# Kernel tuning notes

Measured on AMD Instinct MI355X. Metric: run time of the kernel, lower is better.

The kernel has to match this reference:

```python
import jax, jax.numpy as jnp
from jax import lax
import numpy as np

# dims
B, T, W, D = 8, 24, 48, 512
H = 8            # n_head
E = D // H       # head dim = 64
DI = 2 * D       # mamba d_inner (expand=2) = 1024
S = 64           # d_state
R = 32           # dt_rank = ceil(512/16)
KC = 4           # mamba depthwise conv kernel
DFF = 2048       # ffn hidden
L = T * W


def setup_inputs() -> dict:
    key = jax.random.key(0)
    ks = jax.random.split(key, 32)
    def g(i, shape, s=0.02):
        return jax.random.normal(ks[i], shape, dtype=jnp.float32) * s
    inp = {
        "x": jax.random.normal(ks[0], (B, T, W, D), dtype=jnp.float32),
        "slf_attn_mask": jnp.zeros((B, L), dtype=bool),
        # attention projections (torch Linear convention: y = x @ W.T + b)
        "Wq": g(1, (D, D)), "bq": jnp.zeros((D,), jnp.float32),
        "Wk": g(2, (D, D)), "bk": jnp.zeros((D,), jnp.float32),
        "Wv": g(3, (D, D)), "bv": jnp.zeros((D,), jnp.float32),
        "Wo": g(4, (D, D)), "bo": jnp.zeros((D,), jnp.float32),
        # mamba params
        "in_proj_w": g(5, (2 * DI, D)),
        "conv_w": g(6, (DI, KC), 0.1),
        "conv_b": jnp.zeros((DI,), jnp.float32),
        "x_proj_w": g(7, (R + 2 * S, DI)),
        "dt_proj_w": g(8, (DI, R), 0.1),
        "dt_proj_b": jnp.full((DI,), -3.0, jnp.float32),  # softplus -> small dt
        "A_log": jnp.broadcast_to(jnp.log(jnp.arange(1, S + 1, dtype=jnp.float32)), (DI, S)).copy(),
        "D_ssm": jnp.ones((DI,), jnp.float32),
        "out_proj_w": g(9, (D, DI)),
        # hybrid LayerNorm
        "ln1_g": jnp.ones((D,), jnp.float32), "ln1_b": jnp.zeros((D,), jnp.float32),
        # FFN (pre-norm)
        "ffn_w1": g(10, (DFF, D)), "ffn_b1": jnp.zeros((DFF,), jnp.float32),
        "ffn_w2": g(11, (D, DFF)), "ffn_b2": jnp.zeros((D,), jnp.float32),
        "ln2_g": jnp.ones((D,), jnp.float32), "ln2_b": jnp.zeros((D,), jnp.float32),
    }
    return inp


def _layernorm(x, g, b, eps):
    m = jnp.mean(x, -1, keepdims=True)
    v = jnp.mean(jnp.square(x - m), -1, keepdims=True)
    return (x - m) * lax.rsqrt(v + eps) * g + b


def _attention(xf, mask, Wq, bq, Wk, bk, Wv, bv, Wo, bo):
    # xf: [B, L, D]; mask: [B, L] bool (True = masked)
    b, l, _ = xf.shape
    q = (xf @ Wq.T + bq).reshape(b, l, H, E)
    k = (xf @ Wk.T + bk).reshape(b, l, H, E)
    v = (xf @ Wv.T + bv).reshape(b, l, H, E)
    scale = 1.0 / jnp.sqrt(jnp.float32(E))
    scores = jnp.einsum('blhe,bshe->bhls', q, k)                 # [B,H,L,L]
    scores = jnp.where(mask[:, None, None, :], -jnp.inf, scores)
    probs = jax.nn.softmax(scale * scores, axis=-1)
    out = jnp.einsum('bhls,bshe->blhe', probs, v).reshape(b, l, D)
    return out @ Wo.T + bo


def _mamba(xf, in_proj_w, conv_w, conv_b, x_proj_w, dt_proj_w, dt_proj_b, A_log, D_ssm, out_proj_w):
    # xf: [B, L, D]
    b, l, _ = xf.shape
    xz = xf @ in_proj_w.T                  # [B,L,2*DI]
    u, z = jnp.split(xz, 2, axis=-1)
    # causal depthwise conv1d, kernel KC
    up = jnp.pad(u, ((0, 0), (KC - 1, 0), (0, 0)))
    uc = conv_b + sum(up[:, k:k + l, :] * conv_w[:, k] for k in range(KC))
    u = jax.nn.silu(uc)                    # [B,L,DI]
    xdbc = u @ x_proj_w.T                  # [B,L,R+2S]
    dt_r, Bm, Cm = jnp.split(xdbc, [R, R + S], axis=-1)
    delta = jax.nn.softplus(dt_r @ dt_proj_w.T + dt_proj_b)   # [B,L,DI]
    A = -jnp.exp(A_log)                    # [DI,S]

    def step(h, xs):
        dt_t, u_t, B_t, C_t = xs           # [B,DI],[B,DI],[B,S],[B,S]
        dA = jnp.exp(dt_t[:, :, None] * A)                       # [B,DI,S]
        h = h * dA + (dt_t * u_t)[:, :, None] * B_t[:, None, :]
        y = jnp.einsum('bds,bs->bd', h, C_t)
        return h, y

    xs = (delta.transpose(1, 0, 2), u.transpose(1, 0, 2),
          Bm.transpose(1, 0, 2), Cm.transpose(1, 0, 2))
    h0 = jnp.zeros((b, DI, S), dtype=xf.dtype)
    _, ys = lax.scan(step, h0, xs)
    y = ys.transpose(1, 0, 2) + u * D_ssm  # [B,L,DI]
    y = y * jax.nn.silu(z)
    return y @ out_proj_w.T


def _forward(x, slf_attn_mask, Wq, bq, Wk, bk, Wv, bv, Wo, bo,
             in_proj_w, conv_w, conv_b, x_proj_w, dt_proj_w, dt_proj_b,
             A_log, D_ssm, out_proj_w, ln1_g, ln1_b,
             ffn_w1, ffn_b1, ffn_w2, ffn_b2, ln2_g, ln2_b):
    b, t, w, d = x.shape
    xf = x.reshape(b, t * w, d)
    x_attn = _attention(xf, slf_attn_mask, Wq, bq, Wk, bk, Wv, bv, Wo, bo)
    x_mamba = _mamba(xf, in_proj_w, conv_w, conv_b, x_proj_w, dt_proj_w,
                     dt_proj_b, A_log, D_ssm, out_proj_w)
    h = xf + x_attn + x_mamba
    h = _layernorm(h, ln1_g, ln1_b, 1e-5)
    # pre-norm FFN with residual
    hn = _layernorm(h, ln2_g, ln2_b, 1e-6)
    ff = jax.nn.gelu(hn @ ffn_w1.T + ffn_b1, approximate=False) @ ffn_w2.T + ffn_b2
    out = h + ff
    return out.reshape(b, t, w, d)


def reference(x, slf_attn_mask, Wq, bq, Wk, bk, Wv, bv, Wo, bo,
              in_proj_w, conv_w, conv_b, x_proj_w, dt_proj_w, dt_proj_b,
              A_log, D_ssm, out_proj_w, ln1_g, ln1_b,
              ffn_w1, ffn_b1, ffn_w2, ffn_b2, ln2_g, ln2_b):
    return _forward(x, slf_attn_mask, Wq, bq, Wk, bk, Wv, bv, Wo, bo,
                    in_proj_w, conv_w, conv_b, x_proj_w, dt_proj_w, dt_proj_b,
                    A_log, D_ssm, out_proj_w, ln1_g, ln1_b,
                    ffn_w1, ffn_b1, ffn_w2, ffn_b2, ln2_g, ln2_b)
```

## Files before the change

kernel.cpp:

```cpp
#include <hip/hip_runtime.h>
#include <hip/hip_bf16.h>
#include <math.h>

#define BB 8
#define DD 512
#define HH 8
#define EE 64
#define DI 1024
#define SS 64
#define RR 32
#define KCONV 4
#define DFF 2048
#define LL 1152
#define ML (BB*LL)
#define XS (RR + 2*SS)
#define ZSTR 2048

typedef short bf16x8 __attribute__((ext_vector_type(8)));
typedef float f32x4 __attribute__((ext_vector_type(4)));
typedef unsigned short u16x4 __attribute__((ext_vector_type(4)));

#define GLD_LDS(g, l) \
  __builtin_amdgcn_global_load_lds((const __attribute__((address_space(1))) void*)(g), \
                                   (__attribute__((address_space(3))) void*)(l), 16, 0, 0)

__device__ __forceinline__ float bf2f(unsigned short u) {
  return __uint_as_float(((unsigned)u) << 16);
}

template<int IMM>
__device__ __forceinline__ float swz(float x) {
  return __uint_as_float((unsigned)__builtin_amdgcn_ds_swizzle((int)__float_as_uint(x), IMM));
}

__global__ __launch_bounds__(256) void cvt_bf16(
    const float* __restrict__ s, __hip_bfloat16* __restrict__ d, int n)
{
  const int i = (blockIdx.x * 256 + threadIdx.x) * 4;
  if (i + 3 < n) {
    const float4 v = *(const float4*)(s + i);
    __hip_bfloat16 t[4] = {__float2bfloat16(v.x), __float2bfloat16(v.y),
                           __float2bfloat16(v.z), __float2bfloat16(v.w)};
    *(ushort4*)(d + i) = *(const ushort4*)t;
  } else {
    for (int k = i; k < n; ++k) d[k] = __float2bfloat16(s[k]);
  }
}

__global__ __launch_bounds__(256) void gemm_mfma(
    const __hip_bfloat16* __restrict__ A, int lda,
    const __hip_bfloat16* __restrict__ W,
    const float* __restrict__ bias,
    const float* __restrict__ res,
    void* __restrict__ Cv, void* __restrict__ Cv2,
    int M, int N, int K, int act, int mode)
{
  __shared__ __align__(16) __hip_bfloat16 As[128 * 32];
  __shared__ __align__(16) __hip_bfloat16 Ws[128 * 32];
  const int tid = threadIdx.x;
  const int wid = tid >> 6, lane = tid & 63;
  const int wr = wid >> 1, wc = wid & 1;
  const int m0 = blockIdx.y << 7, n0 = blockIdx.x << 7;
  const int r1 = tid >> 2;
  const int c1 = (tid & 3) << 3;

  const __hip_bfloat16* ga0 = A + (size_t)(m0 + r1) * lda + c1;
  const __hip_bfloat16* ga1 = A + (size_t)(m0 + 64 + r1) * lda + c1;
  const __hip_bfloat16* gw0 = W + (size_t)(n0 + r1) * K + c1;
  const __hip_bfloat16* gw1 = W + (size_t)(n0 + 64 + r1) * K + c1;
  char* lA0 = (char*)As + wid * 1024;
  char* lA1 = lA0 + 4096;
  char* lW0 = (char*)Ws + wid * 1024;
  char* lW1 = lW0 + 4096;

  f32x4 acc[4][4];
#pragma unroll
  for (int i = 0; i < 4; ++i)
#pragma unroll
    for (int j = 0; j < 4; ++j) acc[i][j] = (f32x4){0.f, 0.f, 0.f, 0.f};

  const int fm = lane & 15;
  const int q8 = (lane >> 4) << 3;

  for (int kt = 0; kt < K; kt += 32) {
    __syncthreads();
    GLD_LDS(ga0, lA0); GLD_LDS(ga1, lA1);
    GLD_LDS(gw0, lW0); GLD_LDS(gw1, lW1);
    ga0 += 32; ga1 += 32; gw0 += 32; gw1 += 32;
    __syncthreads();

    bf16x8 af[4], wf[4];
#pragma unroll
    for (int i = 0; i < 4; ++i)
      af[i] = *(const bf16x8*)((const short*)As + (wr * 64 + i * 16 + fm) * 32 + q8);
#pragma unroll
    for (int j = 0; j < 4; ++j)
      wf[j] = *(const bf16x8*)((const short*)Ws + (wc * 64 + j * 16 + fm) * 32 + q8);
#pragma unroll
    for (int i = 0; i < 4; ++i)
#pragma unroll
      for (int j = 0; j < 4; ++j)
        acc[i][j] = __builtin_amdgcn_mfma_f32_16x16x32_bf16(af[i], wf[j], acc[i][j], 0, 0, 0);
  }

  const int rquad = (lane >> 4) << 2;
#pragma unroll
  for (int j = 0; j < 4; ++j) {
    const int n = n0 + wc * 64 + j * 16 + fm;
    if (n < N) {
      const float bv = bias ? bias[n] : 0.f;
#pragma unroll
      for (int i = 0; i < 4; ++i) {
        const int mb = m0 + wr * 64 + i * 16 + rquad;
#pragma unroll
        for (int r = 0; r < 4; ++r) {
          const int m = mb + r;
          float v = acc[i][j][r] + bv;
          if (act == 1) v = 0.5f * v * (1.f + erff(v * 0.70710678118654752f));
          else if (act == 2) v = fmaxf(v, 0.f) + log1pf(expf(-fabsf(v)));
          if (mode == 3) {
            if (n < 1024) {
              ((__hip_bfloat16*)Cv)[(size_t)m * 1024 + n] = __float2bfloat16(v);
            } else {
              const int e = n - 1024;
              const int bb2 = m / LL;
              const int key = m - bb2 * LL;
              ((__hip_bfloat16*)Cv2)[((size_t)(bb2 * HH + (e >> 6)) * EE + (e & 63)) * LL + key] =
                  __float2bfloat16(v);
            }
          } else {
            const size_t off = (size_t)m * N + n;
            if (res) v += res[off];
            if (mode == 1) ((__hip_bfloat16*)Cv)[off] = __float2bfloat16(v);
            else ((float*)Cv)[off] = v;
          }
        }
      }
    }
  }
}

__global__ __launch_bounds__(256) void conv_silu(
    const __hip_bfloat16* __restrict__ xz, const float* __restrict__ cw,
    const float* __restrict__ cb, __hip_bfloat16* __restrict__ uout)
{
  const size_t idx = (size_t)blockIdx.x * 256 + threadIdx.x;
  if (idx >= (size_t)ML * DI) return;
  const int di = (int)(idx & (DI - 1));
  const int row = (int)(idx >> 10);
  const int t = row % LL;
  float acc = cb[di];
#pragma unroll
  for (int k = 0; k < KCONV; ++k) {
    if (t - (KCONV - 1) + k >= 0)
      acc = fmaf((float)xz[(size_t)(row - (KCONV - 1 - k)) * ZSTR + di],
                 cw[di * KCONV + k], acc);
  }
  uout[idx] = __float2bfloat16(acc / (1.f + __expf(-acc)));
}

#define SLOAD(P_, t0_) { _Pragma("unroll") for (int j = 0; j < 4; ++j) { \
    P_##_dt[j] = dp[(size_t)((t0_)+j)*DI]; \
    P_##_u[j]  = bf2f(ubp[(size_t)((t0_)+j)*DI]); \
    P_##_B[j]  = *(const u16x4*)(Bp + (size_t)((t0_)+j)*XS); \
    P_##_C[j]  = *(const u16x4*)(Cp + (size_t)((t0_)+j)*XS); } }

#define SSTEP(P_, j, idx) { \
    const float dtu = P_##_dt[j] * P_##_u[j]; \
    h0 = fmaf(h0, __expf(P_##_dt[j] * Av[0]), dtu * bf2f(P_##_B[j][0])); \
    h1 = fmaf(h1, __expf(P_##_dt[j] * Av[1]), dtu * bf2f(P_##_B[j][1])); \
    h2 = fmaf(h2, __expf(P_##_dt[j] * Av[2]), dtu * bf2f(P_##_B[j][2])); \
    h3 = fmaf(h3, __expf(P_##_dt[j] * Av[3]), dtu * bf2f(P_##_B[j][3])); \
    float part = h0 * bf2f(P_##_C[j][0]); \
    part = fmaf(h1, bf2f(P_##_C[j][1]), part); \
    part = fmaf(h2, bf2f(P_##_C[j][2]), part); \
    part = fmaf(h3, bf2f(P_##_C[j][3]), part); \
    Pp[(idx)] = part; }

#define SCOMP(P_, base_) { \
    SSTEP(P_, 0, (base_)+0) SSTEP(P_, 1, (base_)+1) \
    SSTEP(P_, 2, (base_)+2) SSTEP(P_, 3, (base_)+3) }

__global__ __launch_bounds__(256) void scan_kernel(
    const float* __restrict__ delta, const __hip_bfloat16* __restrict__ ubf,
    const __hip_bfloat16* __restrict__ xz, const __hip_bfloat16* __restrict__ xdbc,
    const float* __restrict__ A_log, const float* __restrict__ D_ssm,
    __hip_bfloat16* __restrict__ y)
{
  const int wv = (int)((blockIdx.x * 256 + threadIdx.x) >> 6);
  const int lane = threadIdx.x & 63;
  const int c = lane >> 4;
  const int s4 = lane & 15;
  const int g = (wv << 2) + c;
  const int b = g >> 10;
  const int di = g & (DI - 1);
  float Av[4];
#pragma unroll
  for (int kk = 0; kk < 4; ++kk)
    Av[kk] = -__expf(A_log[di * SS + (s4 << 2) + kk]);
  const float Dd = D_ssm[di];
  const size_t rb = (size_t)b * LL;
  const float* __restrict__ dp = delta + rb * DI + di;
  const unsigned short* __restrict__ ubp = (const unsigned short*)ubf + rb * DI + di;
  const unsigned short* __restrict__ zbp = (const unsigned short*)xz + rb * ZSTR + DI + di;
  const unsigned short* __restrict__ Bp = (const unsigned short*)xdbc + rb * XS + RR + (s4 << 2);
  const unsigned short* __restrict__ Cp = Bp + SS;
  __hip_bfloat16* __restrict__ yp = y + rb * DI + di;

  float h0 = 0.f, h1 = 0.f, h2 = 0.f, h3 = 0.f;
  float Pp[16];
  float a_dt[4], a_u[4]; u16x4 a_B[4], a_C[4];
  float b_dt[4], b_u[4]; u16x4 b_B[4], b_C[4];
  float c_dt[4], c_u[4]; u16x4 c_B[4], c_C[4];
  float d_dt[4], d_u[4]; u16x4 d_B[4], d_C[4];

  float u_e = bf2f(ubp[(size_t)s4 * DI]);
  float z_e = bf2f(zbp[(size_t)s4 * ZSTR]);

  SLOAD(a, 0) SLOAD(b, 4) SLOAD(c, 8)
  for (int t0 = 0; t0 < LL; t0 += 16) {
    SLOAD(d, t0 + 12)
    SCOMP(a, 0)
    if (t0 + 16 < LL) SLOAD(a, t0 + 16)
    SCOMP(b, 4)
    float u_n = 0.f, z_n = 0.f;
    if (t0 + 16 < LL) {
      u_n = bf2f(ubp[(size_t)(t0 + 16 + s4) * DI]);
      z_n = bf2f(zbp[(size_t)(t0 + 16 + s4) * ZSTR]);
    }
    if (t0 + 20 < LL) SLOAD(b, t0 + 20)
    SCOMP(c, 8)
    if (t0 + 24 < LL) SLOAD(c, t0 + 24)
    SCOMP(d, 12)

#pragma unroll
    for (int k2 = 0; k2 < 8; ++k2) {
      const float mn = (s4 & 1) ? Pp[2*k2+1] : Pp[2*k2];
      const float ot = (s4 & 1) ? Pp[2*k2]   : Pp[2*k2+1];
      Pp[k2] = mn + swz<0x041F>(ot);
    }
#pragma unroll
    for (int k2 = 0; k2 < 4; ++k2) {
      const float mn = (s4 & 2) ? Pp[2*k2+1] : Pp[2*k2];
      const float ot = (s4 & 2) ? Pp[2*k2]   : Pp[2*k2+1];
      Pp[k2] = mn + swz<0x081F>(ot);
    }
#pragma unroll
    for (int k2 = 0; k2 < 2; ++k2) {
      const float mn = (s4 & 4) ? Pp[2*k2+1] : Pp[2*k2];
      const float ot = (s4 & 4) ? Pp[2*k2]   : Pp[2*k2+1];
      Pp[k2] = mn + swz<0x101F>(ot);
    }
    {
      const float mn = (s4 & 8) ? Pp[1] : Pp[0];
      const float ot = (s4 & 8) ? Pp[0] : Pp[1];
      Pp[0] = mn + swz<0x201F>(ot);
    }

    const float yv = (Pp[0] + u_e * Dd) * (z_e / (1.f + __expf(-z_e)));
    yp[(size_t)(t0 + s4) * DI] = __float2bfloat16(yv);
    u_e = u_n; z_e = z_n;
  }
}

__global__ __launch_bounds__(256) void attn_mfma(
    const __hip_bfloat16* __restrict__ qk,
    const __hip_bfloat16* __restrict__ vtg, __hip_bfloat16* __restrict__ og)
{
  __shared__ __align__(16) __hip_bfloat16 Qs[64][72];
  __shared__ __align__(16) __hip_bfloat16 Ks[64][72];
  __shared__ __align__(16) __hip_bfloat16 Vts[64][72];
  __shared__ __align__(16) __hip_bfloat16 Ps[4][16][72];
  const int tid = threadIdx.x;
  const int w = tid >> 6, lane = tid & 63;
  const int bh = blockIdx.y;
  const int b = bh >> 3, hh = bh & 7;
  const int q0 = blockIdx.x << 6;
  const size_t qbase = (size_t)b * LL * 1024 + (size_t)hh * EE;
  const size_t vtbase = (size_t)bh * EE * LL;
  const size_t obase = (size_t)b * LL * DD + (size_t)hh * EE;

  const int srow = tid >> 2, sch = (tid & 3) << 4;
  {
    const __hip_bfloat16* src = qk + qbase + (size_t)(q0 + srow) * 1024 + sch;
    *(uint4*)&Qs[srow][sch]     = *(const uint4*)src;
    *(uint4*)&Qs[srow][sch + 8] = *(const uint4*)(src + 8);
  }
  __syncthreads();

  const int fm = lane & 15;
  const int q8 = (lane >> 4) << 3;
  bf16x8 af0 = *(const bf16x8*)&Qs[w * 16 + fm][q8];
  bf16x8 af1 = *(const bf16x8*)&Qs[w * 16 + fm][32 + q8];

  f32x4 oacc[4];
  float m_i[4], l_i[4];
#pragma unroll
  for (int r = 0; r < 4; ++r) { m_i[r] = -INFINITY; l_i[r] = 0.f; }
#pragma unroll
  for (int j = 0; j < 4; ++j) oacc[j] = (f32x4){0.f, 0.f, 0.f, 0.f};

  for (int kt = 0; kt < LL / 64; ++kt) {
    const int k0 = kt << 6;
    __syncthreads();
    {
      const __hip_bfloat16* ksrc = qk + qbase + 512 + (size_t)(k0 + srow) * 1024 + sch;
      const __hip_bfloat16* vsrc = vtg + vtbase + (size_t)srow * LL + k0 + sch;
      *(uint4*)&Ks[srow][sch]      = *(const uint4*)ksrc;
      *(uint4*)&Ks[srow][sch + 8]  = *(const uint4*)(ksrc + 8);
      *(uint4*)&Vts[srow][sch]     = *(const uint4*)vsrc;
      *(uint4*)&Vts[srow][sch + 8] = *(const uint4*)(vsrc + 8);
    }
    __syncthreads();

    f32x4 sacc[4];
#pragma unroll
    for (int j = 0; j < 4; ++j) sacc[j] = (f32x4){0.f, 0.f, 0.f, 0.f};
#pragma unroll
    for (int j = 0; j < 4; ++j) {
      bf16x8 kf0 = *(const bf16x8*)&Ks[j * 16 + fm][q8];
      bf16x8 kf1 = *(const bf16x8*)&Ks[j * 16 + fm][32 + q8];
      sacc[j] = __builtin_amdgcn_mfma_f32_16x16x32_bf16(af0, kf0, sacc[j], 0, 0, 0);
      sacc[j] = __builtin_amdgcn_mfma_f32_16x16x32_bf16(af1, kf1, sacc[j], 0, 0, 0);
    }

    float alpha[4];
#pragma unroll
    for (int r = 0; r < 4; ++r) {
#pragma unroll
      for (int j = 0; j < 4; ++j) sacc[j][r] *= 0.125f;
      float mt = fmaxf(fmaxf(sacc[0][r], sacc[1][r]), fmaxf(sacc[2][r], sacc[3][r]));
      mt = fmaxf(mt, swz<0x041F>(mt)); mt = fmaxf(mt, swz<0x081F>(mt));
      mt = fmaxf(mt, swz<0x101F>(mt)); mt = fmaxf(mt, swz<0x201F>(mt));
      const float mn = fmaxf(m_i[r], mt);
      alpha[r] = __expf(m_i[r] - mn);
      m_i[r] = mn;
      float p[4], rs = 0.f;
#pragma unroll
      for (int j = 0; j < 4; ++j) { p[j] = __expf(sacc[j][r] - mn); rs += p[j]; }
      rs += swz<0x041F>(rs); rs += swz<0x081F>(rs);
      rs += swz<0x101F>(rs); rs += swz<0x201F>(rs);
      l_i[r] = l_i[r] * alpha[r] + rs;
      const int qrow = ((lane >> 4) << 2) + r;
#pragma unroll
      for (int j = 0; j < 4; ++j)
        Ps[w][qrow][j * 16 + fm] = __float2bfloat16(p[j]);
    }
#pragma unroll
    for (int j = 0; j < 4; ++j)
#pragma unroll
      for (int r = 0; r < 4; ++r) oacc[j][r] *= alpha[r];

    bf16x8 pf0 = *(const bf16x8*)&Ps[w][fm][q8];
    bf16x8 pf1 = *(const bf16x8*)&Ps[w][fm][32 + q8];
#pragma unroll
    for (int j = 0; j < 4; ++j) {
      bf16x8 v0 = *(const bf16x8*)&Vts[j * 16 + fm][q8];
      bf16x8 v1 = *(const bf16x8*)&Vts[j * 16 + fm][32 + q8];
      oacc[j] = __builtin_amdgcn_mfma_f32_16x16x32_bf16(pf0, v0, oacc[j], 0, 0, 0);
      oacc[j] = __builtin_amdgcn_mfma_f32_16x16x32_bf16(pf1, v1, oacc[j], 0, 0, 0);
    }
  }

#pragma unroll
  for (int r = 0; r < 4; ++r) {
    const float inv = 1.f / l_i[r];
    const int qq = q0 + w * 16 + ((lane >> 4) << 2) + r;
#pragma unroll
    for (int j = 0; j < 4; ++j)
      og[obase + (size_t)qq * DD + j * 16 + fm] = __float2bfloat16(oacc[j][r] * inv);
  }
}

__device__ __forceinline__ float block_sum512(float val, float* sm)
{
#pragma unroll
  for (int off = 32; off; off >>= 1) val += __shfl_xor(val, off, 64);
  const int wid = threadIdx.x >> 6;
  __syncthreads();
  if ((threadIdx.x & 63) == 0) sm[wid] = val;
  __syncthreads();
  return sm[0] + sm[1] + sm[2] + sm[3];
}

__global__ __launch_bounds__(256) void ln_fused(
    const float* __restrict__ xf, const float* __restrict__ ao,
    const float* __restrict__ mo,
    const float* __restrict__ g1, const float* __restrict__ b1,
    const float* __restrict__ g2, const float* __restrict__ b2,
    float* __restrict__ hout, __hip_bfloat16* __restrict__ hnout)
{
  __shared__ float sm[4];
  const size_t base = (size_t)blockIdx.x * DD;
  const int t = threadIdx.x;
  const float v0 = xf[base + t] + ao[base + t] + mo[base + t];
  const float v1 = xf[base + 256 + t] + ao[base + 256 + t] + mo[base + 256 + t];
  const float mean = block_sum512(v0 + v1, sm) * (1.f / DD);
  const float d0 = v0 - mean, d1 = v1 - mean;
  const float var = block_sum512(d0 * d0 + d1 * d1, sm) * (1.f / DD);
  const float rstd = rsqrtf(var + 1e-5f);
  const float h0 = d0 * rstd * g1[t] + b1[t];
  const float h1 = d1 * rstd * g1[t + 256] + b1[t + 256];
  hout[base + t] = h0;
  hout[base + 256 + t] = h1;
  const float mean2 = block_sum512(h0 + h1, sm) * (1.f / DD);
  const float e0 = h0 - mean2, e1 = h1 - mean2;
  const float var2 = block_sum512(e0 * e0 + e1 * e1, sm) * (1.f / DD);
  const float rstd2 = rsqrtf(var2 + 1e-6f);
  hnout[base + t] = __float2bfloat16(e0 * rstd2 * g2[t] + b2[t]);
  hnout[base + 256 + t] = __float2bfloat16(e1 * rstd2 * g2[t + 256] + b2[t + 256]);
}

extern "C" void kernel_launch(void* const* d_in, const int* in_sizes, int n_in,
                              void* d_out, int out_size, void* d_ws, size_t ws_size,
                              hipStream_t stream)
{
  const float* x         = (const float*)d_in[0];
  const float* Wq        = (const float*)d_in[2];
  const float* bq        = (const float*)d_in[3];
  const float* Wk        = (const float*)d_in[4];
  const float* bk        = (const float*)d_in[5];
  const float* Wv        = (const float*)d_in[6];
  const float* bv        = (const float*)d_in[7];
  const float* Wo        = (const float*)d_in[8];
  const float* bo        = (const float*)d_in[9];
  const float* in_proj_w = (const float*)d_in[10];
  const float* conv_w    = (const float*)d_in[11];
  const float* conv_b    = (const float*)d_in[12];
  const float* x_proj_w  = (const float*)d_in[13];
  const float* dt_proj_w = (const float*)d_in[14];
  const float* dt_proj_b = (const float*)d_in[15];
  const float* A_log     = (const float*)d_in[16];
  const float* D_ssm     = (const float*)d_in[17];
  const float* out_proj_w= (const float*)d_in[18];
  const float* ln1_g     = (const float*)d_in[19];
  const float* ln1_b     = (const float*)d_in[20];
  const float* ffn_w1    = (const float*)d_in[21];
  const float* ffn_b1    = (const float*)d_in[22];
  const float* ffn_w2    = (const float*)d_in[23];
  const float* ffn_b2    = (const float*)d_in[24];
  const float* ln2_g     = (const float*)d_in[25];
  const float* ln2_b     = (const float*)d_in[26];
  float* out = (float*)d_out;

  float* ws = (float*)d_ws;
  const size_t OF_XBF = 2506752;
  const size_t OF_XZ  = OF_XBF + 2359296;
  const size_t OF_UBF = OF_XZ + 9437184;
  const size_t OF_XD  = OF_UBF + 4718592;
  const size_t OF_DF  = OF_XD + 737280;
  const size_t OF_YB  = OF_DF + 9437184;
  const size_t OF_QB  = OF_YB + 4718592;

  __hip_bfloat16* wbf     = (__hip_bfloat16*)ws;
  __hip_bfloat16* xbf     = (__hip_bfloat16*)(ws + OF_XBF);
  __hip_bfloat16* hnbf    = (__hip_bfloat16*)(ws + OF_XBF);
  __hip_bfloat16* xz      = (__hip_bfloat16*)(ws + OF_XZ);
  __hip_bfloat16* qkbuf   = (__hip_bfloat16*)(ws + OF_XZ);
  __hip_bfloat16* vtbf    = (__hip_bfloat16*)(ws + OF_XZ + 4718592);
  __hip_bfloat16* ubf     = (__hip_bfloat16*)(ws + OF_UBF);
  float*          aobuf   = ws + OF_UBF;
  __hip_bfloat16* xdbc_bf = (__hip_bfloat16*)(ws + OF_XD);
  float*          deltab  = ws + OF_DF;
  __hip_bfloat16* attnbf  = (__hip_bfloat16*)(ws + OF_DF);
  float*          mambab  = ws + OF_DF + 2359296;
  __hip_bfloat16* ffbf    = (__hip_bfloat16*)(ws + OF_DF);
  __hip_bfloat16* ybf     = (__hip_bfloat16*)(ws + OF_YB);
  float*          hbuf    = ws + OF_YB;
  float*          qkvbias = ws + OF_QB;

  const size_t w_inproj = 0;
  const size_t w_xproj  = 1048576;
  const size_t w_dt     = 1310720;
  const size_t w_out    = 1343488;
  const size_t w_q      = 1867776;
  const size_t w_o      = 2654208;
  const size_t w_f1     = 2916352;
  const size_t w_f2     = 3964928;

  const dim3 thr(256);
#define CVT(src, dst, n) cvt_bf16<<<dim3(((n)/4 + 255)/256), thr, 0, stream>>>(src, dst, n)
#define GEMM(Abf, lda_, Woff, Bptr, Rptr, Cptr, C2ptr, N_, K_, act_, md_) \
  gemm_mfma<<<dim3((N_ + 127)/128, ML/128), thr, 0, stream>>>( \
      Abf, lda_, wbf + (Woff), Bptr, Rptr, (void*)(Cptr), (void*)(C2ptr), ML, N_, K_, act_, md_)

  hipMemsetAsync((void*)(wbf + w_xproj + (size_t)160 * 1024), 0, (size_t)96 * 1024 * 2, stream);
  CVT(in_proj_w, wbf + w_inproj, 1048576);
  CVT(x_proj_w,  wbf + w_xproj,  163840);
  CVT(dt_proj_w, wbf + w_dt,     32768);
  CVT(out_proj_w,wbf + w_out,    524288);
  CVT(Wq,        wbf + w_q,           262144);
  CVT(Wk,        wbf + w_q + 262144,  262144);
  CVT(Wv,        wbf + w_q + 524288,  262144);
  CVT(Wo,        wbf + w_o,      262144);
  CVT(ffn_w1,    wbf + w_f1,     1048576);
  CVT(ffn_w2,    wbf + w_f2,     1048576);
  CVT(x,         xbf,            ML * DD);
  hipMemcpyAsync(qkvbias,        bq, 512 * sizeof(float), hipMemcpyDeviceToDevice, stream);
  hipMemcpyAsync(qkvbias + 512,  bk, 512 * sizeof(float), hipMemcpyDeviceToDevice, stream);
  hipMemcpyAsync(qkvbias + 1024, bv, 512 * sizeof(float), hipMemcpyDeviceToDevice, stream);

  GEMM(xbf, DD, w_inproj, nullptr, nullptr, xz, nullptr, 2 * DI, DD, 0, 1);
  conv_silu<<<dim3((ML * DI) / 256), thr, 0, stream>>>(xz, conv_w, conv_b, ubf);
  GEMM(ubf, DI, w_xproj, nullptr, nullptr, xdbc_bf, nullptr, XS, DI, 0, 1);
  GEMM(xdbc_bf, XS, w_dt, dt_proj_b, nullptr, deltab, nullptr, DI, RR, 2, 0);
  scan_kernel<<<dim3(512), thr, 0, stream>>>(
      deltab, ubf, xz, xdbc_bf, A_log, D_ssm, ybf);
  GEMM(ybf, DI, w_out, nullptr, nullptr, mambab, nullptr, DD, DI, 0, 0);

  GEMM(xbf, DD, w_q, qkvbias, nullptr, qkbuf, vtbf, 3 * DD, DD, 0, 3);
  attn_mfma<<<dim3(LL / 64, BB * HH), thr, 0, stream>>>(qkbuf, vtbf, attnbf);
  GEMM(attnbf, DD, w_o, bo, nullptr, aobuf, nullptr, DD, DD, 0, 0);

  ln_fused<<<dim3(ML), thr, 0, stream>>>(x, aobuf, mambab, ln1_g, ln1_b,
                                         ln2_g, ln2_b, hbuf, hnbf);

  GEMM(hnbf, DD, w_f1, ffn_b1, nullptr, ffbf, nullptr, DFF, DD, 1, 1);
  GEMM(ffbf, DFF, w_f2, ffn_b2, hbuf, out, nullptr, DD, DFF, 0, 0);
#undef GEMM
#undef CVT
}
```

Baseline: 1.042 ms.

## Co-launch scan and attention in one kernel and fuse out-proj with Wo GEMM

Merges the selective scan and attention kernels into a single launch whose blocks split by index, so the latency-bound scan (512 blocks) overlaps with attention work. Both write into one concatenated bf16 buffer (mamba y in columns 0-1023, attention output in 1024-1535), letting out_proj and Wo run as one K=1536 GEMM with packed weights; this drops one GEMM and one fp32 intermediate from the LayerNorm input. Delta is now stored in bf16, halving its traffic at some precision cost. The merged kernel carries attention's LDS footprint into scan blocks, which may limit occupancy.

Result: no change. 1.036 ms (-0.6%).

```diff
diff --git a/kernel.cpp b/kernel.cpp
--- a/kernel.cpp
+++ b/kernel.cpp
@@ -15,6 +15,7 @@
 #define ML (BB*LL)
 #define XS (RR + 2*SS)
 #define ZSTR 2048
+#define YSTR 1536
 
 typedef short bf16x8 __attribute__((ext_vector_type(8)));
 typedef float f32x4 __attribute__((ext_vector_type(4)));
@@ -45,6 +46,16 @@
   } else {
     for (int k = i; k < n; ++k) d[k] = __float2bfloat16(s[k]);
   }
+}
+
+__global__ __launch_bounds__(256) void cvt_pack(
+    const float* __restrict__ s, __hip_bfloat16* __restrict__ d,
+    int srclen, int dststride, int dstoff, int total)
+{
+  const int i = blockIdx.x * 256 + threadIdx.x;
+  if (i >= total) return;
+  const int r = i / srclen, c = i - r * srclen;
+  d[(size_t)r * dststride + dstoff + c] = __float2bfloat16(s[i]);
 }
 
 __global__ __launch_bounds__(256) void gemm_mfma(
@@ -160,7 +171,7 @@
 }
 
 #define SLOAD(P_, t0_) { _Pragma("unroll") for (int j = 0; j < 4; ++j) { \
-    P_##_dt[j] = dp[(size_t)((t0_)+j)*DI]; \
+    P_##_dt[j] = bf2f(dp[(size_t)((t0_)+j)*DI]); \
     P_##_u[j]  = bf2f(ubp[(size_t)((t0_)+j)*DI]); \
     P_##_B[j]  = *(const u16x4*)(Bp + (size_t)((t0_)+j)*XS); \
     P_##_C[j]  = *(const u16x4*)(Cp + (size_t)((t0_)+j)*XS); } }
@@ -181,104 +192,105 @@
     SSTEP(P_, 0, (base_)+0) SSTEP(P_, 1, (base_)+1) \
     SSTEP(P_, 2, (base_)+2) SSTEP(P_, 3, (base_)+3) }
 
-__global__ __launch_bounds__(256) void scan_kernel(
-    const float* __restrict__ delta, const __hip_bfloat16* __restrict__ ubf,
+__global__ __launch_bounds__(256) void scan_attn(
+    const __hip_bfloat16* __restrict__ delta, const __hip_bfloat16* __restrict__ ubf,
     const __hip_bfloat16* __restrict__ xz, const __hip_bfloat16* __restrict__ xdbc,
     const float* __restrict__ A_log, const float* __restrict__ D_ssm,
-    __hip_bfloat16* __restrict__ y)
-{
-  const int wv = (int)((blockIdx.x * 256 + threadIdx.x) >> 6);
-  const int lane = threadIdx.x & 63;
-  const int c = lane >> 4;
-  const int s4 = lane & 15;
-  const int g = (wv << 2) + c;
-  const int b = g >> 10;
-  const int di = g & (DI - 1);
-  float Av[4];
-#pragma unroll
-  for (int kk = 0; kk < 4; ++kk)
-    Av[kk] = -__expf(A_log[di * SS + (s4 << 2) + kk]);
-  const float Dd = D_ssm[di];
-  const size_t rb = (size_t)b * LL;
-  const float* __restrict__ dp = delta + rb * DI + di;
-  const unsigned short* __restrict__ ubp = (const unsigned short*)ubf + rb * DI + di;
-  const unsigned short* __restrict__ zbp = (const unsigned short*)xz + rb * ZSTR + DI + di;
-  const unsigned short* __restrict__ Bp = (const unsigned short*)xdbc + rb * XS + RR + (s4 << 2);
-  const unsigned short* __restrict__ Cp = Bp + SS;
-  __hip_bfloat16* __restrict__ yp = y + rb * DI + di;
-
-  float h0 = 0.f, h1 = 0.f, h2 = 0.f, h3 = 0.f;
-  float Pp[16];
-  float a_dt[4], a_u[4]; u16x4 a_B[4], a_C[4];
-  float b_dt[4], b_u[4]; u16x4 b_B[4], b_C[4];
-  float c_dt[4], c_u[4]; u16x4 c_B[4], c_C[4];
-  float d_dt[4], d_u[4]; u16x4 d_B[4], d_C[4];
-
-  float u_e = bf2f(ubp[(size_t)s4 * DI]);
-  float z_e = bf2f(zbp[(size_t)s4 * ZSTR]);
-
-  SLOAD(a, 0) SLOAD(b, 4) SLOAD(c, 8)
-  for (int t0 = 0; t0 < LL; t0 += 16) {
-    SLOAD(d, t0 + 12)
-    SCOMP(a, 0)
-    if (t0 + 16 < LL) SLOAD(a, t0 + 16)
-    SCOMP(b, 4)
-    float u_n = 0.f, z_n = 0.f;
-    if (t0 + 16 < LL) {
-      u_n = bf2f(ubp[(size_t)(t0 + 16 + s4) * DI]);
-      z_n = bf2f(zbp[(size_t)(t0 + 16 + s4) * ZSTR]);
-    }
-    if (t0 + 20 < LL) SLOAD(b, t0 + 20)
-    SCOMP(c, 8)
-    if (t0 + 24 < LL) SLOAD(c, t0 + 24)
-    SCOMP(d, 12)
-
-#pragma unroll
-    for (int k2 = 0; k2 < 8; ++k2) {
-      const float mn = (s4 & 1) ? Pp[2*k2+1] : Pp[2*k2];
-      const float ot = (s4 & 1) ? Pp[2*k2]   : Pp[2*k2+1];
-      Pp[k2] = mn + swz<0x041F>(ot);
-    }
-#pragma unroll
-    for (int k2 = 0; k2 < 4; ++k2) {
-      const float mn = (s4 & 2) ? Pp[2*k2+1] : Pp[2*k2];
-      const float ot = (s4 & 2) ? Pp[2*k2]   : Pp[2*k2+1];
-      Pp[k2] = mn + swz<0x081F>(ot);
-    }
-#pragma unroll
-    for (int k2 = 0; k2 < 2; ++k2) {
-      const float mn = (s4 & 4) ? Pp[2*k2+1] : Pp[2*k2];
-      const float ot = (s4 & 4) ? Pp[2*k2]   : Pp[2*k2+1];
-      Pp[k2] = mn + swz<0x101F>(ot);
-    }
-    {
-      const float mn = (s4 & 8) ? Pp[1] : Pp[0];
-      const float ot = (s4 & 8) ? Pp[0] : Pp[1];
-      Pp[0] = mn + swz<0x201F>(ot);
-    }
-
-    const float yv = (Pp[0] + u_e * Dd) * (z_e / (1.f + __expf(-z_e)));
-    yp[(size_t)(t0 + s4) * DI] = __float2bfloat16(yv);
-    u_e = u_n; z_e = z_n;
-  }
-}
-
-__global__ __launch_bounds__(256) void attn_mfma(
-    const __hip_bfloat16* __restrict__ qk,
-    const __hip_bfloat16* __restrict__ vtg, __hip_bfloat16* __restrict__ og)
+    const __hip_bfloat16* __restrict__ qk, const __hip_bfloat16* __restrict__ vtg,
+    __hip_bfloat16* __restrict__ yattn)
 {
   __shared__ __align__(16) __hip_bfloat16 Qs[64][72];
   __shared__ __align__(16) __hip_bfloat16 Ks[64][72];
   __shared__ __align__(16) __hip_bfloat16 Vts[64][72];
   __shared__ __align__(16) __hip_bfloat16 Ps[4][16][72];
   const int tid = threadIdx.x;
+
+  if (blockIdx.x < 512) {
+    const int wv = (int)((blockIdx.x * 256 + tid) >> 6);
+    const int lane = tid & 63;
+    const int c = lane >> 4;
+    const int s4 = lane & 15;
+    const int g = (wv << 2) + c;
+    const int b = g >> 10;
+    const int di = g & (DI - 1);
+    float Av[4];
+#pragma unroll
+    for (int kk = 0; kk < 4; ++kk)
+      Av[kk] = -__expf(A_log[di * SS + (s4 << 2) + kk]);
+    const float Dd = D_ssm[di];
+    const size_t rb = (size_t)b * LL;
+    const unsigned short* __restrict__ dp = (const unsigned short*)delta + rb * DI + di;
+    const unsigned short* __restrict__ ubp = (const unsigned short*)ubf + rb * DI + di;
+    const unsigned short* __restrict__ zbp = (const unsigned short*)xz + rb * ZSTR + DI + di;
+    const unsigned short* __restrict__ Bp = (const unsigned short*)xdbc + rb * XS + RR + (s4 << 2);
+    const unsigned short* __restrict__ Cp = Bp + SS;
+    __hip_bfloat16* __restrict__ yp = yattn + rb * YSTR + di;
+
+    float h0 = 0.f, h1 = 0.f, h2 = 0.f, h3 = 0.f;
+    float Pp[16];
+    float a_dt[4], a_u[4]; u16x4 a_B[4], a_C[4];
+    float b_dt[4], b_u[4]; u16x4 b_B[4], b_C[4];
+    float c_dt[4], c_u[4]; u16x4 c_B[4], c_C[4];
+    float d_dt[4], d_u[4]; u16x4 d_B[4], d_C[4];
+
+    float u_e = bf2f(ubp[(size_t)s4 * DI]);
+    float z_e = bf2f(zbp[(size_t)s4 * ZSTR]);
+
+    SLOAD(a, 0) SLOAD(b, 4) SLOAD(c, 8)
+    for (int t0 = 0; t0 < LL; t0 += 16) {
+      SLOAD(d, t0 + 12)
+      SCOMP(a, 0)
+      if (t0 + 16 < LL) SLOAD(a, t0 + 16)
+      SCOMP(b, 4)
+      float u_n = 0.f, z_n = 0.f;
+      if (t0 + 16 < LL) {
+        u_n = bf2f(ubp[(size_t)(t0 + 16 + s4) * DI]);
+        z_n = bf2f(zbp[(size_t)(t0 + 16 + s4) * ZSTR]);
+      }
+      if (t0 + 20 < LL) SLOAD(b, t0 + 20)
+      SCOMP(c, 8)
+      if (t0 + 24 < LL) SLOAD(c, t0 + 24)
+      SCOMP(d, 12)
+
+#pragma unroll
+      for (int k2 = 0; k2 < 8; ++k2) {
+        const float mn = (s4 & 1) ? Pp[2*k2+1] : Pp[2*k2];
+        const float ot = (s4 & 1) ? Pp[2*k2]   : Pp[2*k2+1];
+        Pp[k2] = mn + swz<0x041F>(ot);
+      }
+#pragma unroll
+      for (int k2 = 0; k2 < 4; ++k2) {
+        const float mn = (s4 & 2) ? Pp[2*k2+1] : Pp[2*k2];
+        const float ot = (s4 & 2) ? Pp[2*k2]   : Pp[2*k2+1];
+        Pp[k2] = mn + swz<0x081F>(ot);
+      }
+#pragma unroll
+      for (int k2 = 0; k2 < 2; ++k2) {
+        const float mn = (s4 & 4) ? Pp[2*k2+1] : Pp[2*k2];
+        const float ot = (s4 & 4) ? Pp[2*k2]   : Pp[2*k2+1];
+        Pp[k2] = mn + swz<0x101F>(ot);
+      }
+      {
+        const float mn = (s4 & 8) ? Pp[1] : Pp[0];
+        const float ot = (s4 & 8) ? Pp[0] : Pp[1];
+        Pp[0] = mn + swz<0x201F>(ot);
+      }
+
+      const float yv = (Pp[0] + u_e * Dd) * (z_e / (1.f + __expf(-z_e)));
+      yp[(size_t)(t0 + s4) * YSTR] = __float2bfloat16(yv);
+      u_e = u_n; z_e = z_n;
+    }
+    return;
+  }
+
+  const int abid = blockIdx.x - 512;
   const int w = tid >> 6, lane = tid & 63;
-  const int bh = blockIdx.y;
+  const int bh = abid / (LL / 64);
+  const int qtile = abid - bh * (LL / 64);
   const int b = bh >> 3, hh = bh & 7;
-  const int q0 = blockIdx.x << 6;
+  const int q0 = qtile << 6;
   const size_t qbase = (size_t)b * LL * 1024 + (size_t)hh * EE;
   const size_t vtbase = (size_t)bh * EE * LL;
-  const size_t obase = (size_t)b * LL * DD + (size_t)hh * EE;
 
   const int srow = tid >> 2, sch = (tid & 3) << 4;
   {
@@ -368,7 +380,8 @@
     const int qq = q0 + w * 16 + ((lane >> 4) << 2) + r;
 #pragma unroll
     for (int j = 0; j < 4; ++j)
-      og[obase + (size_t)qq * DD + j * 16 + fm] = __float2bfloat16(oacc[j][r] * inv);
+      yattn[((size_t)b * LL + qq) * YSTR + 1024 + hh * EE + j * 16 + fm] =
+          __float2bfloat16(oacc[j][r] * inv);
   }
 }
 
@@ -384,8 +397,7 @@
 }
 
 __global__ __launch_bounds__(256) void ln_fused(
-    const float* __restrict__ xf, const float* __restrict__ ao,
-    const float* __restrict__ mo,
+    const float* __restrict__ xf, const float* __restrict__ combo,
     const float* __restrict__ g1, const float* __restrict__ b1,
     const float* __restrict__ g2, const float* __restrict__ b2,
     float* __restrict__ hout, __hip_bfloat16* __restrict__ hnout)
@@ -393,8 +405,8 @@
   __shared__ float sm[4];
   const size_t base = (size_t)blockIdx.x * DD;
   const int t = threadIdx.x;
-  const float v0 = xf[base + t] + ao[base + t] + mo[base + t];
-  const float v1 = xf[base + 256 + t] + ao[base + 256 + t] + mo[base + 256 + t];
+  const float v0 = xf[base + t] + combo[base + t];
+  const float v1 = xf[base + 256 + t] + combo[base + 256 + t];
   const float mean = block_sum512(v0 + v1, sm) * (1.f / DD);
   const float d0 = v0 - mean, d1 = v1 - mean;
   const float var = block_sum512(d0 * d0 + d1 * d1, sm) * (1.f / DD);
@@ -449,32 +461,30 @@
   const size_t OF_UBF = OF_XZ + 9437184;
   const size_t OF_XD  = OF_UBF + 4718592;
   const size_t OF_DF  = OF_XD + 737280;
-  const size_t OF_YB  = OF_DF + 9437184;
-  const size_t OF_QB  = OF_YB + 4718592;
+  const size_t OF_QKV = OF_DF + 4718592;
+  const size_t OF_YA  = OF_QKV + 7077888;
+  const size_t OF_QB  = OF_YA + 7077888;
 
   __hip_bfloat16* wbf     = (__hip_bfloat16*)ws;
   __hip_bfloat16* xbf     = (__hip_bfloat16*)(ws + OF_XBF);
   __hip_bfloat16* hnbf    = (__hip_bfloat16*)(ws + OF_XBF);
   __hip_bfloat16* xz      = (__hip_bfloat16*)(ws + OF_XZ);
-  __hip_bfloat16* qkbuf   = (__hip_bfloat16*)(ws + OF_XZ);
-  __hip_bfloat16* vtbf    = (__hip_bfloat16*)(ws + OF_XZ + 4718592);
   __hip_bfloat16* ubf     = (__hip_bfloat16*)(ws + OF_UBF);
-  float*          aobuf   = ws + OF_UBF;
+  float*          combo   = ws + OF_UBF;
   __hip_bfloat16* xdbc_bf = (__hip_bfloat16*)(ws + OF_XD);
-  float*          deltab  = ws + OF_DF;
-  __hip_bfloat16* attnbf  = (__hip_bfloat16*)(ws + OF_DF);
-  float*          mambab  = ws + OF_DF + 2359296;
+  __hip_bfloat16* deltab  = (__hip_bfloat16*)(ws + OF_DF);
   __hip_bfloat16* ffbf    = (__hip_bfloat16*)(ws + OF_DF);
-  __hip_bfloat16* ybf     = (__hip_bfloat16*)(ws + OF_YB);
-  float*          hbuf    = ws + OF_YB;
+  __hip_bfloat16* qkbuf   = (__hip_bfloat16*)(ws + OF_QKV);
+  __hip_bfloat16* vtbf    = (__hip_bfloat16*)(ws + OF_QKV + 4718592);
+  __hip_bfloat16* yattn   = (__hip_bfloat16*)(ws + OF_YA);
+  float*          hbuf    = ws + OF_YA;
   float*          qkvbias = ws + OF_QB;
 
   const size_t w_inproj = 0;
   const size_t w_xproj  = 1048576;
   const size_t w_dt     = 1310720;
-  const size_t w_out    = 1343488;
-  const size_t w_q      = 1867776;
-  const size_t w_o      = 2654208;
+  const size_t w_cat    = 1343488;
+  const size_t w_q      = 2129920;
   const size_t w_f1     = 2916352;
   const size_t w_f2     = 3964928;
 
@@ -488,14 +498,16 @@
   CVT(in_proj_w, wbf + w_inproj, 1048576);
   CVT(x_proj_w,  wbf + w_xproj,  163840);
   CVT(dt_proj_w, wbf + w_dt,     32768);
-  CVT(out_proj_w,wbf + w_out,    524288);
+  cvt_pack<<<dim3((524288 + 255)/256), thr, 0, stream>>>(
+      out_proj_w, wbf + w_cat, 1024, 1536, 0,    524288);
+  cvt_pack<<<dim3((262144 + 255)/256), thr, 0, stream>>>(
+      Wo,         wbf + w_cat, 512,  1536, 1024, 262144);
   CVT(Wq,        wbf + w_q,           262144);
   CVT(Wk,        wbf + w_q + 262144,  262144);
   CVT(Wv,        wbf + w_q + 524288,  262144);
-  CVT(Wo,        wbf + w_o,      262144);
-  CVT(ffn_w1,    wbf + w_f1,     1048576);
-  CVT(ffn_w2,    wbf + w_f2,     1048576);
-  CVT(x,         xbf,            ML * DD);
+  CVT(ffn_w1,    wbf + w_f1,    1048576);
+  CVT(ffn_w2,    wbf + w_f2,    1048576);
+  CVT(x,         xbf,           ML * DD);
   hipMemcpyAsync(qkvbias,        bq, 512 * sizeof(float), hipMemcpyDeviceToDevice, stream);
   hipMemcpyAsync(qkvbias + 512,  bk, 512 * sizeof(float), hipMemcpyDeviceToDevice, stream);
   hipMemcpyAsync(qkvbias + 1024, bv, 512 * sizeof(float), hipMemcpyDeviceToDevice, stream);
@@ -503,16 +515,16 @@
   GEMM(xbf, DD, w_inproj, nullptr, nullptr, xz, nullptr, 2 * DI, DD, 0, 1);
   conv_silu<<<dim3((ML * DI) / 256), thr, 0, stream>>>(xz, conv_w, conv_b, ubf);
   GEMM(ubf, DI, w_xproj, nullptr, nullptr, xdbc_bf, nullptr, XS, DI, 0, 1);
-  GEMM(xdbc_bf, XS, w_dt, dt_proj_b, nullptr, deltab, nullptr, DI, RR, 2, 0);
-  scan_kernel<<<dim3(512), thr, 0, stream>>>(
-      deltab, ubf, xz, xdbc_bf, A_log, D_ssm, ybf);
-  GEMM(ybf, DI, w_out, nullptr, nullptr, mambab, nullptr, DD, DI, 0, 0);
+  GEMM(xdbc_bf, XS, w_dt, dt_proj_b, nullptr, deltab, nullptr, DI, RR, 2, 1);
 
   GEMM(xbf, DD, w_q, qkvbias, nullptr, qkbuf, vtbf, 3 * DD, DD, 0, 3);
-  attn_mfma<<<dim3(LL / 64, BB * HH), thr, 0, stream>>>(qkbuf, vtbf, attnbf);
-  GEMM(attnbf, DD, w_o, bo, nullptr, aobuf, nullptr, DD, DD, 0, 0);
-
-  ln_fused<<<dim3(ML), thr, 0, stream>>>(x, aobuf, mambab, ln1_g, ln1_b,
+
+  scan_attn<<<dim3(512 + BB * HH * (LL / 64)), thr, 0, stream>>>(
+      deltab, ubf, xz, xdbc_bf, A_log, D_ssm, qkbuf, vtbf, yattn);
+
+  GEMM(yattn, YSTR, w_cat, bo, nullptr, combo, nullptr, DD, YSTR, 0, 0);
+
+  ln_fused<<<dim3(ML), thr, 0, stream>>>(x, combo, ln1_g, ln1_b,
                                          ln2_g, ln2_b, hbuf, hnbf);
 
   GEMM(hnbf, DD, w_f1, ffn_b1, nullptr, ffbf, nullptr, DFF, DD, 1, 1);
```
